# Optimization experiments

Measured on AMD Instinct MI355X. Metric: run time of the kernel, lower is better.

## Reference

```python
import jax, jax.numpy as jnp
import numpy as np

EPS = 1e-12  # torch F.normalize eps

def _l2norm(x):
    n = jnp.linalg.norm(x, axis=1, keepdims=True)
    return x / jnp.maximum(n, EPS)

def setup_inputs() -> dict:
    key = jax.random.key(0)
    kq, km = jax.random.split(key)
    queries = jax.random.normal(kq, (4096, 128), dtype=jnp.float32)
    memory = jax.random.normal(km, (100000, 128), dtype=jnp.float32)
    return {"queries": queries, "memory": memory, "k": 3}

def reference(queries, memory, k):
    q = _l2norm(queries)                      # [N, D]
    m = _l2norm(memory)                       # [M, D]
    sims = q @ m.T                            # [N, M]
    values, indices = jax.lax.top_k(sims, k)  # [N, k] each
    distances = 1.0 - values
    return distances, indices
```

## Files before the change

kernel.cpp:

```cpp
#include <hip/hip_runtime.h>
#include <hip/hip_bf16.h>

typedef unsigned short u16;
typedef unsigned int u32;

#define N_Q 4096
#define N_M 100000
#define N_M_PAD 100096
#define DDIM 128
#define QTILE 256
#define MTILE 64
#define NCHUNK 32
#define NQT (N_Q / QTILE)
#define TOTAL_MT (N_M_PAD / MTILE)
#define TPC ((TOTAL_MT + NCHUNK - 1) / NCHUNK)
#define NCAND (NCHUNK * 2 * 3)

typedef short bf16x8 __attribute__((ext_vector_type(8)));
typedef float f32x4 __attribute__((ext_vector_type(4)));

static __device__ __forceinline__ u16 f2bf(float v) {
  union { float f; u32 u; } a; a.f = v;
  u32 r = a.u + 0x7fffu + ((a.u >> 16) & 1u);
  return (u16)(r >> 16);
}

static __device__ __forceinline__ void async_copy16(const u16* gp, u16* lp) {
  __builtin_amdgcn_global_load_lds(
      (const __attribute__((address_space(1))) u32*)gp,
      (__attribute__((address_space(3))) u32*)lp, 16, 0, 0);
}

__global__ __launch_bounds__(256) void knorm(const float* __restrict__ q, const float* __restrict__ m,
                                             u16* __restrict__ qn, u16* __restrict__ mn,
                                             float* __restrict__ qinv, float* __restrict__ minv) {
  const int lane = threadIdx.x & 63;
  const int nw = gridDim.x * 4;
  for (int row = blockIdx.x * 4 + (threadIdx.x >> 6); row < N_Q + N_M_PAD; row += nw) {
    const float* src;
    u16* dst;
    int mr = 0;
    bool is_q = (row < N_Q);
    bool pad = false;
    if (is_q) {
      src = q + (size_t)row * DDIM;
      dst = qn + (size_t)row * DDIM;
    } else {
      mr = row - N_Q;
      pad = (mr >= N_M);
      src = m + (size_t)mr * DDIM;
      dst = mn + (size_t)mr * DDIM;
    }
    float2 x;
    if (pad) { x.x = 0.f; x.y = 0.f; }
    else x = ((const float2*)src)[lane];
    float s = x.x * x.x + x.y * x.y;
    #pragma unroll
    for (int off = 1; off < 64; off <<= 1) s += __shfl_xor(s, off, 64);
    float invn = 1.0f / fmaxf(sqrtf(s), 1e-12f);
    u32 packed = (u32)f2bf(x.x * invn) | ((u32)f2bf(x.y * invn) << 16);
    ((u32*)dst)[lane] = packed;
    if (lane == 0) {
      if (is_q) qinv[row] = invn;
      else minv[mr] = pad ? 0.f : invn;
    }
  }
}

static __device__ __forceinline__ void stage2(const u16* __restrict__ mn, u16* dst,
                                              int t, const u32* goff, u32 loff0) {
  const u16* gbase = mn + (size_t)t * MTILE * DDIM;
  #pragma unroll
  for (int it = 0; it < 2; ++it)
    async_copy16(gbase + goff[it], dst + loff0 + (u32)(it * 64) * 8);
}

static __device__ __forceinline__ void tileWork(
    const u16* As, int tl, int wm, int quad, int l15,
    const bf16x8 (&bq)[4][4], float (&tv0)[4], float (&tv1)[4], float (&tv2)[4]) {
  f32x4 acc[2][4];
  __builtin_amdgcn_s_setprio(1);
  {
    int c = quad ^ l15;
    bf16x8 a0 = *(const bf16x8*)&As[((wm * 32 + l15) * 16 + c) * 8];
    bf16x8 a1 = *(const bf16x8*)&As[((wm * 32 + 16 + l15) * 16 + c) * 8];
    f32x4 z = {0.f, 0.f, 0.f, 0.f};
    #pragma unroll
    for (int ni = 0; ni < 4; ++ni) {
      acc[0][ni] = __builtin_amdgcn_mfma_f32_16x16x32_bf16(a0, bq[ni][0], z, 0, 0, 0);
      acc[1][ni] = __builtin_amdgcn_mfma_f32_16x16x32_bf16(a1, bq[ni][0], z, 0, 0, 0);
    }
  }
  #pragma unroll
  for (int s = 1; s < 4; ++s) {
    int c = (s * 4 + quad) ^ l15;
    bf16x8 a0 = *(const bf16x8*)&As[((wm * 32 + l15) * 16 + c) * 8];
    bf16x8 a1 = *(const bf16x8*)&As[((wm * 32 + 16 + l15) * 16 + c) * 8];
    #pragma unroll
    for (int ni = 0; ni < 4; ++ni) {
      acc[0][ni] = __builtin_amdgcn_mfma_f32_16x16x32_bf16(a0, bq[ni][s], acc[0][ni], 0, 0, 0);
      acc[1][ni] = __builtin_amdgcn_mfma_f32_16x16x32_bf16(a1, bq[ni][s], acc[1][ni], 0, 0, 0);
    }
  }
  __builtin_amdgcn_s_setprio(0);
  const u32 code = ((u32)tl << 2) | (u32)quad;
  #pragma unroll
  for (int ni = 0; ni < 4; ++ni) {
    f32x4 x0 = acc[0][ni], x1 = acc[1][ni];
    float M = fmaxf(fmaxf(fmaxf(x0[0], x0[1]), fmaxf(x0[2], x0[3])),
                    fmaxf(fmaxf(x1[0], x1[1]), fmaxf(x1[2], x1[3])));
    float pk = __uint_as_float((__float_as_uint(M) & 0xFFFFFE00u) | code);
    tv2[ni] = __builtin_amdgcn_fmed3f(tv1[ni], tv2[ni], pk);
    tv1[ni] = __builtin_amdgcn_fmed3f(tv0[ni], tv1[ni], pk);
    tv0[ni] = fmaxf(tv0[ni], pk);
  }
}

__global__ __launch_bounds__(512, 4) void kgemm(const u16* __restrict__ qn,
                                                const u16* __restrict__ mn,
                                                float* __restrict__ pval) {
  __shared__ u16 B0[MTILE * DDIM];
  __shared__ u16 B1[MTILE * DDIM];
  __shared__ u16 B2[MTILE * DDIM];
  __shared__ u16 B3[MTILE * DDIM];

  const int id = blockIdx.x;
  const int xcd = id & 7, sub = id >> 3;
  const int ch = xcd * 4 + (sub >> 4);
  const int qt = sub & 15;
  const int tid = threadIdx.x;
  const int wid = tid >> 6, lane = tid & 63;
  const int quad = lane >> 4, l15 = lane & 15;
  const int wm = wid >> 2, wq = wid & 3;

  const int t0 = ch * TPC;
  const int t1 = (t0 + TPC < TOTAL_MT) ? (t0 + TPC) : TOTAL_MT;
  const int nt = t1 - t0;

  u32 goff[2];
  u32 loff0;
  {
    int u0 = wid * 128 + lane;
    loff0 = (u32)(wid * 128) * 8;
    #pragma unroll
    for (int it = 0; it < 2; ++it) {
      int u = u0 + it * 64;
      int row = u >> 4, su = u & 15;
      int k8 = su ^ (row & 15);
      goff[it] = (u32)(row * DDIM + k8 * 8);
    }
  }

  stage2(mn, B0, t0 + 0, goff, loff0);
  stage2(mn, B1, t0 + 1, goff, loff0);
  stage2(mn, B2, t0 + 2, goff, loff0);

  bf16x8 bq[4][4];
  #pragma unroll
  for (int ni = 0; ni < 4; ++ni) {
    int col = qt * QTILE + wq * 64 + ni * 16 + l15;
    #pragma unroll
    for (int s = 0; s < 4; ++s)
      bq[ni][s] = *(const bf16x8*)&qn[(size_t)col * DDIM + (s * 4 + quad) * 8];
  }

  float tv0[4], tv1[4], tv2[4];
  #pragma unroll
  for (int i = 0; i < 4; ++i) { tv0[i] = tv1[i] = tv2[i] = -1e30f; }

  asm volatile("s_waitcnt vmcnt(0)" ::: "memory");
  asm volatile("s_barrier" ::: "memory");

  int r = 0;
  #define ROUND(BC, BS)                                                        \
    {                                                                          \
      int ts = t0 + r + 3;                                                     \
      ts = (ts < t1) ? ts : (t1 - 1);                                          \
      stage2(mn, BS, ts, goff, loff0);                                         \
      tileWork(BC, r, wm, quad, l15, bq, tv0, tv1, tv2);                       \
      asm volatile("s_waitcnt vmcnt(4)" ::: "memory");                         \
      asm volatile("s_barrier" ::: "memory");                                  \
      ++r;                                                                     \
      if (r >= nt) break;                                                      \
    }
  while (true) {
    ROUND(B0, B3)
    ROUND(B1, B0)
    ROUND(B2, B1)
    ROUND(B3, B2)
  }
  #undef ROUND

  #pragma unroll
  for (int ni = 0; ni < 4; ++ni) {
    float a0 = tv0[ni], a1 = tv1[ni], a2 = tv2[ni];
    #pragma unroll
    for (int off = 16; off <= 32; off <<= 1) {
      float b0 = __shfl_xor(a0, off, 64);
      float b1 = __shfl_xor(a1, off, 64);
      float b2 = __shfl_xor(a2, off, 64);
      float n0 = fmaxf(a0, b0);
      float n1 = __builtin_amdgcn_fmed3f(a0, b0, fmaxf(a1, b1));
      float n2 = fmaxf(fmaxf(fminf(a1, b0), fminf(a0, b1)), fmaxf(a2, b2));
      a0 = n0; a1 = n1; a2 = n2;
    }
    float v = (quad == 0) ? a0 : ((quad == 1) ? a1 : a2);
    if (quad < 3) {
      int qlocal = wq * 64 + ni * 16 + l15;
      size_t base = (((size_t)qt * NCHUNK + ch) * QTILE + qlocal) * 6 + wm * 3 + quad;
      pval[base] = v;
    }
  }
}

__global__ __launch_bounds__(256) void kmerge(const float* __restrict__ pval,
                                              const float* __restrict__ q,
                                              const float* __restrict__ mem,
                                              const float* __restrict__ qinv,
                                              const float* __restrict__ minv,
                                              float* __restrict__ out) {
  __shared__ float sv[4][64];
  const int tid = threadIdx.x;
  const int wq = tid >> 6;
  const int lane = tid & 63;
  const int qg = blockIdx.x * 4 + wq;
  const int qt = qg >> 8, ql = qg & 255;

  const int c0 = lane * 3;
  float cv[3];
  {
    int chn = c0 / 6, rem = c0 - chn * 6;
    size_t b = (((size_t)qt * NCHUNK + chn) * QTILE + ql) * 6 + rem;
    cv[0] = pval[b];
    cv[1] = pval[b + 1];
    cv[2] = pval[b + 2];
  }

  float wv[8]; int wp[8];
  #pragma unroll
  for (int pass = 0; pass < 8; ++pass) {
    float bv = cv[0]; int bp = c0;
    if (cv[1] > bv) { bv = cv[1]; bp = c0 + 1; }
    if (cv[2] > bv) { bv = cv[2]; bp = c0 + 2; }
    #pragma unroll
    for (int off = 32; off >= 1; off >>= 1) {
      float ov = __shfl_xor(bv, off, 64);
      int op = __shfl_xor(bp, off, 64);
      bool g = (ov > bv) || (ov == bv && op < bp);
      bv = g ? ov : bv; bp = g ? op : bp;
    }
    wv[pass] = bv; wp[pass] = bp;
    int d = bp - c0;
    if (d == 0) cv[0] = -1e31f;
    if (d == 1) cv[1] = -1e31f;
    if (d == 2) cv[2] = -1e31f;
  }

  const float qi = qinv[qg];
  const float* qrow = q + (size_t)qg * DDIM;
  const int e = lane >> 3, f = lane & 7;

  #pragma unroll
  for (int p = 0; p < 8; ++p) {
    int bp = wp[p];
    u32 code = __float_as_uint(wv[p]) & 511u;
    int chn = bp / 6;
    int wm = (bp - chn * 6) / 3;
    int tl = (int)(code >> 2), qd = (int)(code & 3u);
    int row = (chn * TPC + tl) * MTILE + wm * 32 + (e >> 2) * 16 + qd * 4 + (e & 3);
    bool valid = (row < N_M);
    int ra = valid ? row : 0;
    const float* mrow = mem + (size_t)ra * DDIM;
    float s = 0.f;
    #pragma unroll
    for (int i = 0; i < 4; ++i) {
      float4 mv = *(const float4*)&mrow[(f + 8 * i) * 4];
      float4 qv = *(const float4*)&qrow[(f + 8 * i) * 4];
      s += qv.x * mv.x + qv.y * mv.y + qv.z * mv.z + qv.w * mv.w;
    }
    #pragma unroll
    for (int off = 1; off < 8; off <<= 1) s += __shfl_xor(s, off, 64);
    s = valid ? (s * qi * minv[ra]) : -1e30f;
    if (f == 0) sv[wq][p * 8 + e] = s;
  }
  __syncthreads();

  float myv = sv[wq][lane];
  {
    int p = lane >> 3, e2 = lane & 7;
    int bp = wp[p];
    u32 code = __float_as_uint(wv[p]) & 511u;
    int chn = bp / 6;
    int wm = (bp - chn * 6) / 3;
    int tl = (int)(code >> 2), qd = (int)(code & 3u);
    int row = (chn * TPC + tl) * MTILE + wm * 32 + (e2 >> 2) * 16 + qd * 4 + (e2 & 3);
    int myrow = (row < N_M) ? row : (N_M + lane);

    #pragma unroll
    for (int a = 0; a < 3; ++a) {
      float bv = myv; int bi = myrow;
      #pragma unroll
      for (int off = 32; off >= 1; off >>= 1) {
        float ov = __shfl_xor(bv, off, 64);
        int oi = __shfl_xor(bi, off, 64);
        bool g2 = (ov > bv) || (ov == bv && oi < bi);
        bv = g2 ? ov : bv; bi = g2 ? oi : bi;
      }
      if (lane == 0) {
        out[(size_t)qg * 3 + a] = 1.0f - bv;
        out[(size_t)N_Q * 3 + (size_t)qg * 3 + a] = (float)bi;
      }
      if (myrow == bi) myv = -1e31f;
    }
  }
}

extern "C" void kernel_launch(void* const* d_in, const int* in_sizes, int n_in,
                              void* d_out, int out_size, void* d_ws, size_t ws_size,
                              hipStream_t stream) {
  const float* q = (const float*)d_in[0];
  const float* m = (const float*)d_in[1];

  char* ws = (char*)d_ws;
  size_t off = 0;
  u16* qn = (u16*)(ws + off); off += (size_t)N_Q * DDIM * 2;
  u16* mn = (u16*)(ws + off); off += (size_t)N_M_PAD * DDIM * 2;
  float* qinv = (float*)(ws + off); off += (size_t)N_Q * 4;
  float* minv = (float*)(ws + off); off += (size_t)N_M_PAD * 4;
  float* pval = (float*)(ws + off); off += (size_t)N_Q * NCAND * 4;

  knorm<<<1024, 256, 0, stream>>>(q, m, qn, mn, qinv, minv);
  kgemm<<<NQT * NCHUNK, 512, 0, stream>>>(qn, mn, pval);
  kmerge<<<N_Q / 4, 256, 0, stream>>>(pval, q, m, qinv, minv, (float*)d_out);
}
```

Before: 214.2 us.

## Process tile pairs per barrier and stage partial top-k output through LDS

The main loop now stages two tiles per round and computes on two previously loaded tiles before a single full wait and barrier, which halves the number of barriers per tile. The output of the per-chunk top-3 candidates is first written to shared memory and then copied out with coalesced float4 stores instead of scattered scalar stores. The price is shallower prefetch: the full vmcnt(0) wait each round can expose memory latency that the old three-tile-ahead ring buffer hid.

```diff
diff --git a/kernel.cpp b/kernel.cpp
--- a/kernel.cpp
+++ b/kernel.cpp
@@ -153,7 +153,6 @@
 
   stage2(mn, B0, t0 + 0, goff, loff0);
   stage2(mn, B1, t0 + 1, goff, loff0);
-  stage2(mn, B2, t0 + 2, goff, loff0);
 
   bf16x8 bq[4][4];
   #pragma unroll
@@ -171,26 +170,27 @@
   asm volatile("s_waitcnt vmcnt(0)" ::: "memory");
   asm volatile("s_barrier" ::: "memory");
 
-  int r = 0;
-  #define ROUND(BC, BS)                                                        \
+  int u = 0;
+  #define SROUND(Ba, Bb, Bc, Bd)                                               \
     {                                                                          \
-      int ts = t0 + r + 3;                                                     \
-      ts = (ts < t1) ? ts : (t1 - 1);                                          \
-      stage2(mn, BS, ts, goff, loff0);                                         \
-      tileWork(BC, r, wm, quad, l15, bq, tv0, tv1, tv2);                       \
-      asm volatile("s_waitcnt vmcnt(4)" ::: "memory");                         \
+      int ta = t0 + u + 2, tb = t0 + u + 3;                                    \
+      if (ta < t1) stage2(mn, Bc, ta, goff, loff0);                            \
+      if (tb < t1) stage2(mn, Bd, tb, goff, loff0);                            \
+      tileWork(Ba, u, wm, quad, l15, bq, tv0, tv1, tv2);                       \
+      if (u + 1 < nt) tileWork(Bb, u + 1, wm, quad, l15, bq, tv0, tv1, tv2);   \
+      u += 2;                                                                  \
+      if (u >= nt) break;                                                      \
+      asm volatile("s_waitcnt vmcnt(0)" ::: "memory");                         \
       asm volatile("s_barrier" ::: "memory");                                  \
-      ++r;                                                                     \
-      if (r >= nt) break;                                                      \
     }
   while (true) {
-    ROUND(B0, B3)
-    ROUND(B1, B0)
-    ROUND(B2, B1)
-    ROUND(B3, B2)
-  }
-  #undef ROUND
-
+    SROUND(B0, B1, B2, B3)
+    SROUND(B2, B3, B0, B1)
+  }
+  #undef SROUND
+
+  __syncthreads();
+  float* sout = (float*)B0;
   #pragma unroll
   for (int ni = 0; ni < 4; ++ni) {
     float a0 = tv0[ni], a1 = tv1[ni], a2 = tv2[ni];
@@ -207,9 +207,14 @@
     float v = (quad == 0) ? a0 : ((quad == 1) ? a1 : a2);
     if (quad < 3) {
       int qlocal = wq * 64 + ni * 16 + l15;
-      size_t base = (((size_t)qt * NCHUNK + ch) * QTILE + qlocal) * 6 + wm * 3 + quad;
-      pval[base] = v;
-    }
+      sout[qlocal * 6 + wm * 3 + quad] = v;
+    }
+  }
+  __syncthreads();
+  {
+    const size_t pbase = ((size_t)qt * NCHUNK + ch) * QTILE * 6;
+    if (tid < 384)
+      ((float4*)(pval + pbase))[tid] = ((const float4*)sout)[tid];
   }
 }
 
```

New measurement: 232.8 us. +8.7%, slower.
